# Performance work log

Hardware: AMD Instinct MI355X
Metric: run time of the kernel (lower is better)

Reference implementation:

```python
import jax, jax.numpy as jnp
import numpy as np

B, N, C = 2, 2048, 768
H = 12
HD = C // H
SCALE = HD ** -0.5


def setup_inputs() -> dict:
    key = jax.random.key(0)
    ks = jax.random.split(key, 5)
    s = 1.0 / np.sqrt(C)
    return {
        "x": jax.random.normal(ks[0], (B, N, C), dtype=jnp.float32),
        "Wq": jax.random.normal(ks[1], (C, C), dtype=jnp.float32) * s,
        "Wk": jax.random.normal(ks[2], (C, C), dtype=jnp.float32) * s,
        "Wv": jax.random.normal(ks[3], (C, C), dtype=jnp.float32) * s,
        "Wo": jax.random.normal(ks[4], (C, C), dtype=jnp.float32) * s,
        "bo": jnp.zeros((C,), dtype=jnp.float32),
    }


def reference(x, Wq, Wk, Wv, Wo, bo):
    b, n, c = x.shape
    # projections (equinox Linear: y = W @ x, i.e. x @ W.T); split heads -> [b, h, n, hd]
    q = (x @ Wq.T).reshape(b, n, H, HD).transpose(0, 2, 1, 3)
    k = (x @ Wk.T).reshape(b, n, H, HD).transpose(0, 2, 1, 3)
    v = (x @ Wv.T).reshape(b, n, H, HD).transpose(0, 2, 1, 3)
    # full O(N^2) score matrix, scaled dot-product
    scores = jnp.einsum("bhqd,bhkd->bhqk", q, k) * SCALE  # [b, h, n, n]
    probs = jax.nn.softmax(scores, axis=-1)
    # attn_drop = 0.0 -> identity
    out = jnp.einsum("bhqk,bhkd->bhqd", probs, v)  # [b, h, n, hd]
    out = out.transpose(0, 2, 1, 3).reshape(b, n, c)
    # output projection (proj_drop = 0.0 -> identity)
    return out @ Wo.T + bo
```

## Files before the change

kernel.cpp:

```cpp
#include <hip/hip_runtime.h>
#include <hip/hip_bf16.h>
#include <cstdint>

typedef __bf16 bf16;
typedef bf16 bf16x8 __attribute__((ext_vector_type(8)));
typedef float f32x4 __attribute__((ext_vector_type(4)));
typedef uint32_t u32;

#define MFMA16(a, b, c) __builtin_amdgcn_mfma_f32_16x16x32_bf16(a, b, c, 0, 0, 0)

static constexpr int Bb = 2, Hh = 12, Nn = 2048, Cc = 768, HD = 64;
static constexpr float SCALE_L2E = 0.125f * 1.4426950408889634f;

__device__ inline u32 pkbf(float a, float b) {
    union { struct { uint16_t lo, hi; } s; u32 w; } u;
    u.s.lo = __builtin_bit_cast(uint16_t, (bf16)a);
    u.s.hi = __builtin_bit_cast(uint16_t, (bf16)b);
    return u.w;
}

__device__ __forceinline__ size_t fidx(int bh, int n, int hd) {
    return ((size_t)(bh * 128 + (n >> 4)) * 2 + (hd >> 5)) * 512 +
           (size_t)(((hd >> 3) & 3) * 128 + (n & 15) * 8 + (hd & 7));
}
__device__ __forceinline__ size_t vidx(int bh, int n, int hd) {
    return (((size_t)(bh * 32 + (n >> 6)) * 4 + (hd >> 4)) * 2 + ((n >> 5) & 1)) * 512 +
           (size_t)(((n >> 3) & 3) * 128 + (hd & 15) * 8 + (n & 7));
}

__device__ __forceinline__ void stage16(const bf16* g, bf16* l) {
    __builtin_amdgcn_global_load_lds(
        (const __attribute__((address_space(1))) void*)g,
        (__attribute__((address_space(3))) void*)l, 16, 0, 0);
}

#define VMWAIT(N) do { asm volatile("s_waitcnt vmcnt(" #N ")" ::); \
                       __builtin_amdgcn_sched_barrier(0); } while (0)

#define GLD(dst, addr, off) \
    asm volatile("global_load_dwordx4 %0, %1, off offset:" #off \
                 : "=v"(dst) : "v"(addr))

#define CVTPK(w, a, b) \
    asm("v_cvt_pk_bf16_f32 %0, %1, %2" : "=v"(w) : "v"(a), "v"(b))

__global__ __launch_bounds__(256) void cvt_all(const float* __restrict__ x,
                                               const float* __restrict__ wq,
                                               const float* __restrict__ wk,
                                               const float* __restrict__ wv,
                                               const float* __restrict__ wo,
                                               bf16* __restrict__ xb,
                                               bf16* __restrict__ wqkv,
                                               bf16* __restrict__ wob) {
    const int b = blockIdx.x;
    const float* src;
    bf16* dst;
    int i;
    if (b < 1536) {
        src = x; dst = xb; i = b * 256 + threadIdx.x;
    } else {
        const int wbid  = b - 1536;
        const int which = wbid / 288;
        src = which == 0 ? wq : which == 1 ? wk : which == 2 ? wv : wo;
        dst = which == 3 ? wob : wqkv + (size_t)which * 589824;
        i = (wbid % 288) * 256 + threadIdx.x;
    }
    const float4* p = reinterpret_cast<const float4*>(src) + (size_t)i * 2;
    float4 v0 = p[0], v1 = p[1];
    bf16x8 o;
    o[0] = (bf16)v0.x; o[1] = (bf16)v0.y; o[2] = (bf16)v0.z; o[3] = (bf16)v0.w;
    o[4] = (bf16)v1.x; o[5] = (bf16)v1.y; o[6] = (bf16)v1.z; o[7] = (bf16)v1.w;
    reinterpret_cast<bf16x8*>(dst)[i] = o;
}

__global__ __launch_bounds__(256, 3) void gemm_qkv(const bf16* __restrict__ X,
                                                   const bf16* __restrict__ W,
                                                   bf16* __restrict__ QF,
                                                   bf16* __restrict__ KF,
                                                   bf16* __restrict__ VF) {
    const int m0      = blockIdx.x * 128;
    const int j00     = blockIdx.y * 128;
    const int grp     = blockIdx.y / 6;
    const int colbase = (blockIdx.y % 6) * 128;
    const int w   = threadIdx.x >> 6;
    const int wr  = w >> 1;
    const int wc  = w & 1;
    const int l   = threadIdx.x & 63;
    const int lr  = l & 15;
    const int lg  = l >> 4;

    __shared__ bf16 lsA[2][128 * 32];
    __shared__ bf16 lsB[2][128 * 32];

    const int lrow = l >> 2;
    const int lcol = (l & 3) * 8;

    auto STAGE = [&](int buf, int kk) {
#pragma unroll
        for (int i = 0; i < 2; i++) {
            const int s = w * 2 + i;
            stage16(X + (size_t)(m0 + s * 16 + lrow) * Cc + kk + lcol, &lsA[buf][s * 512]);
            stage16(W + (size_t)(j00 + s * 16 + lrow) * Cc + kk + lcol, &lsB[buf][s * 512]);
        }
    };

    f32x4 acc[4][4] = {};

    STAGE(0, 0);
    __syncthreads();
    int cur = 0;
#pragma unroll 1
    for (int it = 0; it < 24; ++it) {
        if (it < 23) STAGE(cur ^ 1, (it + 1) * 32);
        bf16x8 a[4], b[4];
#pragma unroll
        for (int r = 0; r < 4; r++)
            a[r] = *reinterpret_cast<const bf16x8*>(&lsA[cur][(wr * 64 + r * 16 + lr) * 32 + lg * 8]);
#pragma unroll
        for (int c = 0; c < 4; c++)
            b[c] = *reinterpret_cast<const bf16x8*>(&lsB[cur][(wc * 64 + c * 16 + lr) * 32 + lg * 8]);
        __builtin_amdgcn_s_setprio(1);
#pragma unroll
        for (int r = 0; r < 4; r++)
#pragma unroll
            for (int c = 0; c < 4; c++)
                acc[r][c] = MFMA16(a[r], b[c], acc[r][c]);
        __builtin_amdgcn_s_setprio(0);
        __syncthreads();
        cur ^= 1;
    }

#pragma unroll
    for (int r = 0; r < 4; r++)
#pragma unroll
        for (int c = 0; c < 4; c++)
#pragma unroll
            for (int j = 0; j < 4; j++) {
                const int m   = m0 + wr * 64 + r * 16 + lg * 4 + j;
                const int col = colbase + wc * 64 + c * 16 + lr;
                const int bb = m >> 11, n = m & 2047;
                const int h = col >> 6, hd = col & 63;
                const int bh = bb * Hh + h;
                const float v = acc[r][c][j];
                if (grp == 0) {
                    QF[fidx(bh, n, hd)] = (bf16)(v * SCALE_L2E);
                } else if (grp == 1) {
                    KF[fidx(bh, n, hd)] = (bf16)v;
                } else {
                    VF[vidx(bh, n, hd)] = (bf16)v;
                }
            }
}

__global__ __launch_bounds__(256) void gemm_proj(const bf16* __restrict__ X,
                                                 const bf16* __restrict__ W,
                                                 const float* __restrict__ bias,
                                                 float* __restrict__ Y) {
    const int m0 = blockIdx.x * 64;
    const int j0 = blockIdx.y * 64;
    const int w  = threadIdx.x >> 6;
    const int l  = threadIdx.x & 63;
    const int lr = l & 15;
    const int lg = l >> 4;

    __shared__ bf16 lsA[2][64 * 32];
    __shared__ bf16 lsB[2][64 * 32];

    const int lrow = l >> 2;
    const int lcol = (l & 3) * 8;

    auto STAGE = [&](int buf, int kk) {
        stage16(X + (size_t)(m0 + w * 16 + lrow) * Cc + kk + lcol, &lsA[buf][w * 512]);
        stage16(W + (size_t)(j0 + w * 16 + lrow) * Cc + kk + lcol, &lsB[buf][w * 512]);
    };

    f32x4 acc[4] = {};

    STAGE(0, 0);
    __syncthreads();
    int cur = 0;
#pragma unroll 1
    for (int it = 0; it < 24; ++it) {
        if (it < 23) STAGE(cur ^ 1, (it + 1) * 32);
        bf16x8 a = *reinterpret_cast<const bf16x8*>(&lsA[cur][(w * 16 + lr) * 32 + lg * 8]);
        bf16x8 b[4];
#pragma unroll
        for (int c = 0; c < 4; c++)
            b[c] = *reinterpret_cast<const bf16x8*>(&lsB[cur][(c * 16 + lr) * 32 + lg * 8]);
        __builtin_amdgcn_s_setprio(1);
#pragma unroll
        for (int c = 0; c < 4; c++)
            acc[c] = MFMA16(a, b[c], acc[c]);
        __builtin_amdgcn_s_setprio(0);
        __syncthreads();
        cur ^= 1;
    }

    const int mw = m0 + w * 16;
#pragma unroll
    for (int c = 0; c < 4; c++)
#pragma unroll
        for (int j = 0; j < 4; j++) {
            const int m   = mw + lg * 4 + j;
            const int col = j0 + c * 16 + lr;
            Y[(size_t)m * Cc + col] = acc[c][j] + bias[col];
        }
}

__global__ __launch_bounds__(256, 2) void attn_kernel(const bf16* __restrict__ QF,
                                                      const bf16* __restrict__ KF,
                                                      const bf16* __restrict__ VF,
                                                      bf16* __restrict__ AO) {
    const int bid  = (blockIdx.x & 7) * 96 + (blockIdx.x >> 3);
    const int qb   = bid & 31;
    const int bh   = bid >> 5;
    const int tid  = threadIdx.x;
    const int wid  = tid >> 6;
    const int team = wid >> 1;
    const int wt   = wid & 1;
    const int l    = tid & 63;
    const int lr   = l & 15;
    const int lg   = l >> 4;

    __shared__ u32 p_lds[4][2][576];

    f32x4 acc[2][4] = {};
    f32x4 accs[2] = {};

    const bf16* Qbase = QF + ((size_t)(bh * 128 + qb * 4 + wt * 2) * 2) * 512 + l * 8;
    const bf16x8 qa0 = *reinterpret_cast<const bf16x8*>(Qbase);
    const bf16x8 qb0 = *reinterpret_cast<const bf16x8*>(Qbase + 512);
    const bf16x8 qa1 = *reinterpret_cast<const bf16x8*>(Qbase + 1024);
    const bf16x8 qb1 = *reinterpret_cast<const bf16x8*>(Qbase + 1536);

    bf16x8 ONES;
#pragma unroll
    for (int i = 0; i < 8; i++) ONES[i] = (bf16)1.0f;

    bf16x8 ka[8], vv[8];
    const int tbase = team * 16;

    const bf16* kA = KF + ((size_t)bh * 256 + tbase * 8) * 512 + l * 8;
    const bf16* kB = kA + 2048;
    const bf16* vA = VF + ((size_t)bh * 256 + tbase * 8) * 512 + l * 8;
    const bf16* vB = vA + 2048;

    auto loadK = [&]() {
        GLD(ka[0], kA, 0);
        GLD(ka[1], kA, 1024);
        GLD(ka[2], kA, 2048);
        GLD(ka[3], kA, 3072);
        GLD(ka[4], kB, 0);
        GLD(ka[5], kB, 1024);
        GLD(ka[6], kB, 2048);
        GLD(ka[7], kB, 3072);
    };
    auto loadV = [&]() {
        GLD(vv[0], vA, 0);
        GLD(vv[1], vA, 1024);
        GLD(vv[2], vA, 2048);
        GLD(vv[3], vA, 3072);
        GLD(vv[4], vB, 0);
        GLD(vv[5], vB, 1024);
        GLD(vv[6], vB, 2048);
        GLD(vv[7], vB, 3072);
    };

    const f32x4 fz = {0.f, 0.f, 0.f, 0.f};

    auto EXPPACK = [&](int f, const f32x4* s) {
#pragma unroll
        for (int st = 0; st < 4; st++) {
            float e0 = exp2f(s[st][0]);
            float e1 = exp2f(s[st][1]);
            float e2 = exp2f(s[st][2]);
            float e3 = exp2f(s[st][3]);
            u32 w0, w1;
            CVTPK(w0, e0, e1);
            CVTPK(w1, e2, e3);
            *reinterpret_cast<uint2*>(&p_lds[wid][f][lr * 36 + st * 8 + lg * 2]) =
                make_uint2(w0, w1);
        }
    };

    loadK();
    loadV();

#pragma unroll 1
    for (int t = 0; t < 16; ++t) {
        VMWAIT(8);

        f32x4 s[4];
        __builtin_amdgcn_s_setprio(1);
#pragma unroll
        for (int st = 0; st < 4; st++) {
            s[st] = MFMA16(ka[st * 2], qa0, fz);
            s[st] = MFMA16(ka[st * 2 + 1], qb0, s[st]);
        }
        __builtin_amdgcn_s_setprio(0);
        EXPPACK(0, s);
        __builtin_amdgcn_s_setprio(1);
#pragma unroll
        for (int st = 0; st < 4; st++) {
            s[st] = MFMA16(ka[st * 2], qa1, fz);
            s[st] = MFMA16(ka[st * 2 + 1], qb1, s[st]);
        }
        __builtin_amdgcn_s_setprio(0);
        if (t < 15) {
            kA += 4096; kB += 4096;
            loadK();
        }
        EXPPACK(1, s);

        asm volatile("s_waitcnt lgkmcnt(0)" ::: "memory");
        __builtin_amdgcn_sched_barrier(0);
        const bf16x8 pa00 = *reinterpret_cast<const bf16x8*>(&p_lds[wid][0][lr * 36 + lg * 4]);
        const bf16x8 pa01 = *reinterpret_cast<const bf16x8*>(&p_lds[wid][0][lr * 36 + 16 + lg * 4]);
        const bf16x8 pa10 = *reinterpret_cast<const bf16x8*>(&p_lds[wid][1][lr * 36 + lg * 4]);
        const bf16x8 pa11 = *reinterpret_cast<const bf16x8*>(&p_lds[wid][1][lr * 36 + 16 + lg * 4]);

        VMWAIT(8);
        __builtin_amdgcn_s_setprio(1);
#pragma unroll
        for (int c = 0; c < 4; c++) {
            acc[0][c] = MFMA16(vv[c * 2], pa00, acc[0][c]);
            acc[0][c] = MFMA16(vv[c * 2 + 1], pa01, acc[0][c]);
            acc[1][c] = MFMA16(vv[c * 2], pa10, acc[1][c]);
            acc[1][c] = MFMA16(vv[c * 2 + 1], pa11, acc[1][c]);
        }
        accs[0] = MFMA16(ONES, pa00, accs[0]);
        accs[0] = MFMA16(ONES, pa01, accs[0]);
        accs[1] = MFMA16(ONES, pa10, accs[1]);
        accs[1] = MFMA16(ONES, pa11, accs[1]);
        __builtin_amdgcn_s_setprio(0);
        if (t < 15) {
            vA += 4096; vB += 4096;
            loadV();
        }
    }

    __syncthreads();
    float* mrg = reinterpret_cast<float*>(&p_lds[0][0][0]);
    if (team == 1) {
#pragma unroll
        for (int f = 0; f < 2; f++) {
            float* slot = mrg + (wt * 2 + f) * 1088 + l * 17;
#pragma unroll
            for (int c = 0; c < 4; c++)
#pragma unroll
                for (int j = 0; j < 4; j++) slot[c * 4 + j] = acc[f][c][j];
            slot[16] = accs[f][0];
        }
    }
    __syncthreads();
    if (team == 1) return;

    const int bb = bh / Hh, h = bh % Hh;
#pragma unroll
    for (int f = 0; f < 2; f++) {
        const float* slot = mrg + (wt * 2 + f) * 1088 + l * 17;
#pragma unroll
        for (int c = 0; c < 4; c++)
#pragma unroll
            for (int j = 0; j < 4; j++) acc[f][c][j] += slot[c * 4 + j];
        const float rtot = accs[f][0] + slot[16];
        const float rinv = 1.0f / rtot;
        asm volatile("s_waitcnt lgkmcnt(0)" ::: "memory");
        __builtin_amdgcn_sched_barrier(0);

        float* o_lds = mrg + (wt * 2 + f) * 1088;
#pragma unroll
        for (int c = 0; c < 4; c++)
#pragma unroll
            for (int j = 0; j < 4; j++)
                o_lds[(c * 16 + lg * 4 + j) * 17 + lr] = acc[f][c][j] * rinv;
        asm volatile("s_waitcnt lgkmcnt(0)" ::: "memory");
        __builtin_amdgcn_sched_barrier(0);

        const int q0 = qb * 64 + (wt * 2 + f) * 16;
        const int qq = l >> 2, dc = (l & 3) * 16;
        bf16x8 o0, o1;
#pragma unroll
        for (int dd = 0; dd < 8; dd++) o0[dd] = (bf16)o_lds[(dc + dd) * 17 + qq];
#pragma unroll
        for (int dd = 0; dd < 8; dd++) o1[dd] = (bf16)o_lds[(dc + 8 + dd) * 17 + qq];
        bf16* dst = AO + ((size_t)(bb * Nn) + q0 + qq) * Cc + h * 64 + dc;
        *reinterpret_cast<bf16x8*>(dst) = o0;
        *reinterpret_cast<bf16x8*>(dst + 8) = o1;
    }
}

extern "C" void kernel_launch(void* const* d_in, const int* in_sizes, int n_in,
                              void* d_out, int out_size, void* d_ws, size_t ws_size,
                              hipStream_t stream) {
    const float* x  = (const float*)d_in[0];
    const float* Wq = (const float*)d_in[1];
    const float* Wk = (const float*)d_in[2];
    const float* Wv = (const float*)d_in[3];
    const float* Wo = (const float*)d_in[4];
    const float* bo = (const float*)d_in[5];

    const size_t XB    = 0;
    const size_t WQKVB = XB + 6291456;
    const size_t WOB   = WQKVB + 3538944;
    const size_t QB    = WOB + 1179648;
    const size_t KB    = QB + 6291456;
    const size_t VTB   = KB + 6291456;
    const size_t AOB   = VTB + 6291456;
    const size_t NEED  = AOB + 6291456;
    if (ws_size < NEED) return;

    char* ws = (char*)d_ws;
    bf16* xb   = (bf16*)(ws + XB);
    bf16* wqkv = (bf16*)(ws + WQKVB);
    bf16* wob  = (bf16*)(ws + WOB);
    bf16* QF   = (bf16*)(ws + QB);
    bf16* KF   = (bf16*)(ws + KB);
    bf16* VF   = (bf16*)(ws + VTB);
    bf16* AOb  = (bf16*)(ws + AOB);

    cvt_all<<<2688, 256, 0, stream>>>(x, Wq, Wk, Wv, Wo, xb, wqkv, wob);

    gemm_qkv<<<dim3(32, 18), 256, 0, stream>>>(xb, wqkv, QF, KF, VF);

    attn_kernel<<<768, 256, 0, stream>>>(QF, KF, VF, AOb);

    gemm_proj<<<dim3(64, 12), 256, 0, stream>>>(AOb, wob, bo, (float*)d_out);
}
```

Baseline: 91.80 us.

## Switch attention to 32x32x16 MFMA and keep P in registers via permlane swap

Moves the attention kernel from 16x16x32 MFMA tiles to 32x32x16 tiles, rewriting the Q/K/V fragment layouts produced by the QKV GEMM. The exponentiated scores are packed to bf16 and rearranged across lane halves with v_permlane32_swap, so the P operand goes straight into the PV MFMA instead of round-tripping through LDS. The aim is to drop the per-iteration LDS writes, reads and waits and use fewer, larger MFMAs. The cost is higher register pressure from 16-wide accumulators, and correctness now rests on the new layout and swap mapping being exactly right.

```diff
diff --git a/kernel.cpp b/kernel.cpp
--- a/kernel.cpp
+++ b/kernel.cpp
@@ -5,27 +5,23 @@
 typedef __bf16 bf16;
 typedef bf16 bf16x8 __attribute__((ext_vector_type(8)));
 typedef float f32x4 __attribute__((ext_vector_type(4)));
+typedef float f32x16 __attribute__((ext_vector_type(16)));
 typedef uint32_t u32;
+typedef u32 u32x4 __attribute__((ext_vector_type(4)));
 
 #define MFMA16(a, b, c) __builtin_amdgcn_mfma_f32_16x16x32_bf16(a, b, c, 0, 0, 0)
+#define MFMA32(a, b, c) __builtin_amdgcn_mfma_f32_32x32x16_bf16(a, b, c, 0, 0, 0)
 
 static constexpr int Bb = 2, Hh = 12, Nn = 2048, Cc = 768, HD = 64;
 static constexpr float SCALE_L2E = 0.125f * 1.4426950408889634f;
 
-__device__ inline u32 pkbf(float a, float b) {
-    union { struct { uint16_t lo, hi; } s; u32 w; } u;
-    u.s.lo = __builtin_bit_cast(uint16_t, (bf16)a);
-    u.s.hi = __builtin_bit_cast(uint16_t, (bf16)b);
-    return u.w;
-}
-
-__device__ __forceinline__ size_t fidx(int bh, int n, int hd) {
-    return ((size_t)(bh * 128 + (n >> 4)) * 2 + (hd >> 5)) * 512 +
-           (size_t)(((hd >> 3) & 3) * 128 + (n & 15) * 8 + (hd & 7));
-}
-__device__ __forceinline__ size_t vidx(int bh, int n, int hd) {
-    return (((size_t)(bh * 32 + (n >> 6)) * 4 + (hd >> 4)) * 2 + ((n >> 5) & 1)) * 512 +
-           (size_t)(((n >> 3) & 3) * 128 + (hd & 15) * 8 + (n & 7));
+__device__ __forceinline__ size_t fidx32(int bh, int n, int hd) {
+    return ((size_t)(bh * 64 + (n >> 5)) * 4 + (hd >> 4)) * 512 +
+           (size_t)(((((hd >> 3) & 1) << 5) + (n & 31)) * 8 + (hd & 7));
+}
+__device__ __forceinline__ size_t vidx32(int bh, int n, int hd) {
+    return (((size_t)(bh * 32 + (n >> 6)) * 2 + (hd >> 5)) * 4 + ((n >> 4) & 3)) * 512 +
+           (size_t)(((((n >> 3) & 1) << 5) + (hd & 31)) * 8 + (n & 7));
 }
 
 __device__ __forceinline__ void stage16(const bf16* g, bf16* l) {
@@ -43,6 +39,9 @@
 
 #define CVTPK(w, a, b) \
     asm("v_cvt_pk_bf16_f32 %0, %1, %2" : "=v"(w) : "v"(a), "v"(b))
+
+#define PLSWAP(a, b) \
+    asm("v_permlane32_swap_b32 %0, %1" : "+v"(a), "+v"(b))
 
 __global__ __launch_bounds__(256) void cvt_all(const float* __restrict__ x,
                                                const float* __restrict__ wq,
@@ -143,11 +142,11 @@
                 const int bh = bb * Hh + h;
                 const float v = acc[r][c][j];
                 if (grp == 0) {
-                    QF[fidx(bh, n, hd)] = (bf16)(v * SCALE_L2E);
+                    QF[fidx32(bh, n, hd)] = (bf16)(v * SCALE_L2E);
                 } else if (grp == 1) {
-                    KF[fidx(bh, n, hd)] = (bf16)v;
+                    KF[fidx32(bh, n, hd)] = (bf16)v;
                 } else {
-                    VF[vidx(bh, n, hd)] = (bf16)v;
+                    VF[vidx32(bh, n, hd)] = (bf16)v;
                 }
             }
 }
@@ -219,19 +218,19 @@
     const int team = wid >> 1;
     const int wt   = wid & 1;
     const int l    = tid & 63;
-    const int lr   = l & 15;
-    const int lg   = l >> 4;
-
-    __shared__ u32 p_lds[4][2][576];
-
-    f32x4 acc[2][4] = {};
-    f32x4 accs[2] = {};
-
-    const bf16* Qbase = QF + ((size_t)(bh * 128 + qb * 4 + wt * 2) * 2) * 512 + l * 8;
-    const bf16x8 qa0 = *reinterpret_cast<const bf16x8*>(Qbase);
-    const bf16x8 qb0 = *reinterpret_cast<const bf16x8*>(Qbase + 512);
-    const bf16x8 qa1 = *reinterpret_cast<const bf16x8*>(Qbase + 1024);
-    const bf16x8 qb1 = *reinterpret_cast<const bf16x8*>(Qbase + 1536);
+    const int q    = l & 31;
+    const int hi   = l >> 5;
+
+    __shared__ float mrg[4224];
+
+    f32x16 acc0 = {}, acc1 = {};
+    f32x16 accs = {};
+
+    const bf16* Qp = QF + ((size_t)(bh * 64 + qb * 2 + wt) * 4) * 512 + l * 8;
+    bf16x8 qf[4];
+#pragma unroll
+    for (int dc = 0; dc < 4; dc++)
+        qf[dc] = *reinterpret_cast<const bf16x8*>(Qp + dc * 512);
 
     bf16x8 ONES;
 #pragma unroll
@@ -266,20 +265,24 @@
         GLD(vv[7], vB, 3072);
     };
 
-    const f32x4 fz = {0.f, 0.f, 0.f, 0.f};
-
-    auto EXPPACK = [&](int f, const f32x4* s) {
-#pragma unroll
-        for (int st = 0; st < 4; st++) {
-            float e0 = exp2f(s[st][0]);
-            float e1 = exp2f(s[st][1]);
-            float e2 = exp2f(s[st][2]);
-            float e3 = exp2f(s[st][3]);
-            u32 w0, w1;
-            CVTPK(w0, e0, e1);
-            CVTPK(w1, e2, e3);
-            *reinterpret_cast<uint2*>(&p_lds[wid][f][lr * 36 + st * 8 + lg * 2]) =
-                make_uint2(w0, w1);
+    const f32x16 fz16 = {};
+
+    auto BUILDB = [&](const f32x16& sP, bf16x8* Bw) {
+        float e[16];
+#pragma unroll
+        for (int r = 0; r < 16; r++) e[r] = exp2f(sP[r]);
+#pragma unroll
+        for (int c2 = 0; c2 < 2; c2++) {
+            u32 x0, x1, y0, y1;
+            CVTPK(x0, e[8 * c2 + 0], e[8 * c2 + 1]);
+            CVTPK(x1, e[8 * c2 + 2], e[8 * c2 + 3]);
+            CVTPK(y0, e[8 * c2 + 4], e[8 * c2 + 5]);
+            CVTPK(y1, e[8 * c2 + 6], e[8 * c2 + 7]);
+            PLSWAP(x0, y0);
+            PLSWAP(x1, y1);
+            u32x4 wv4;
+            wv4[0] = x0; wv4[1] = x1; wv4[2] = y0; wv4[3] = y1;
+            Bw[c2] = __builtin_bit_cast(bf16x8, wv4);
         }
     };
 
@@ -290,48 +293,32 @@
     for (int t = 0; t < 16; ++t) {
         VMWAIT(8);
 
-        f32x4 s[4];
+        bf16x8 Bw[4];
         __builtin_amdgcn_s_setprio(1);
-#pragma unroll
-        for (int st = 0; st < 4; st++) {
-            s[st] = MFMA16(ka[st * 2], qa0, fz);
-            s[st] = MFMA16(ka[st * 2 + 1], qb0, s[st]);
-        }
+        f32x16 s0 = fz16;
+#pragma unroll
+        for (int dc = 0; dc < 4; dc++) s0 = MFMA32(ka[dc], qf[dc], s0);
         __builtin_amdgcn_s_setprio(0);
-        EXPPACK(0, s);
+        BUILDB(s0, &Bw[0]);
         __builtin_amdgcn_s_setprio(1);
-#pragma unroll
-        for (int st = 0; st < 4; st++) {
-            s[st] = MFMA16(ka[st * 2], qa1, fz);
-            s[st] = MFMA16(ka[st * 2 + 1], qb1, s[st]);
-        }
+        f32x16 s1 = fz16;
+#pragma unroll
+        for (int dc = 0; dc < 4; dc++) s1 = MFMA32(ka[4 + dc], qf[dc], s1);
         __builtin_amdgcn_s_setprio(0);
         if (t < 15) {
             kA += 4096; kB += 4096;
             loadK();
         }
-        EXPPACK(1, s);
-
-        asm volatile("s_waitcnt lgkmcnt(0)" ::: "memory");
-        __builtin_amdgcn_sched_barrier(0);
-        const bf16x8 pa00 = *reinterpret_cast<const bf16x8*>(&p_lds[wid][0][lr * 36 + lg * 4]);
-        const bf16x8 pa01 = *reinterpret_cast<const bf16x8*>(&p_lds[wid][0][lr * 36 + 16 + lg * 4]);
-        const bf16x8 pa10 = *reinterpret_cast<const bf16x8*>(&p_lds[wid][1][lr * 36 + lg * 4]);
-        const bf16x8 pa11 = *reinterpret_cast<const bf16x8*>(&p_lds[wid][1][lr * 36 + 16 + lg * 4]);
-
-        VMWAIT(8);
+        BUILDB(s1, &Bw[2]);
+
+        if (t < 15) { VMWAIT(8); } else { VMWAIT(0); }
         __builtin_amdgcn_s_setprio(1);
 #pragma unroll
-        for (int c = 0; c < 4; c++) {
-            acc[0][c] = MFMA16(vv[c * 2], pa00, acc[0][c]);
-            acc[0][c] = MFMA16(vv[c * 2 + 1], pa01, acc[0][c]);
-            acc[1][c] = MFMA16(vv[c * 2], pa10, acc[1][c]);
-            acc[1][c] = MFMA16(vv[c * 2 + 1], pa11, acc[1][c]);
-        }
-        accs[0] = MFMA16(ONES, pa00, accs[0]);
-        accs[0] = MFMA16(ONES, pa01, accs[0]);
-        accs[1] = MFMA16(ONES, pa10, accs[1]);
-        accs[1] = MFMA16(ONES, pa11, accs[1]);
+        for (int kc = 0; kc < 4; kc++) {
+            acc0 = MFMA32(vv[kc], Bw[kc], acc0);
+            acc1 = MFMA32(vv[4 + kc], Bw[kc], acc1);
+            accs = MFMA32(ONES, Bw[kc], accs);
+        }
         __builtin_amdgcn_s_setprio(0);
         if (t < 15) {
             vA += 4096; vB += 4096;
@@ -340,53 +327,41 @@
     }
 
     __syncthreads();
-    float* mrg = reinterpret_cast<float*>(&p_lds[0][0][0]);
+    float* slot = mrg + wt * 2112 + l * 33;
     if (team == 1) {
 #pragma unroll
-        for (int f = 0; f < 2; f++) {
-            float* slot = mrg + (wt * 2 + f) * 1088 + l * 17;
-#pragma unroll
-            for (int c = 0; c < 4; c++)
-#pragma unroll
-                for (int j = 0; j < 4; j++) slot[c * 4 + j] = acc[f][c][j];
-            slot[16] = accs[f][0];
-        }
+        for (int r = 0; r < 16; r++) { slot[r] = acc0[r]; slot[16 + r] = acc1[r]; }
+        slot[32] = accs[0];
     }
     __syncthreads();
     if (team == 1) return;
 
+#pragma unroll
+    for (int r = 0; r < 16; r++) { acc0[r] += slot[r]; acc1[r] += slot[16 + r]; }
+    const float rinv = 1.0f / (accs[0] + slot[32]);
+    asm volatile("s_waitcnt lgkmcnt(0)" ::: "memory");
+    __builtin_amdgcn_sched_barrier(0);
+
+    float* o_lds = mrg + wt * 2112;
+#pragma unroll
+    for (int r = 0; r < 16; r++) {
+        const int d = (r & 3) + 8 * (r >> 2) + 4 * hi;
+        o_lds[d * 33 + q] = acc0[r] * rinv;
+        o_lds[(d + 32) * 33 + q] = acc1[r] * rinv;
+    }
+    asm volatile("s_waitcnt lgkmcnt(0)" ::: "memory");
+    __builtin_amdgcn_sched_barrier(0);
+
     const int bb = bh / Hh, h = bh % Hh;
-#pragma unroll
-    for (int f = 0; f < 2; f++) {
-        const float* slot = mrg + (wt * 2 + f) * 1088 + l * 17;
-#pragma unroll
-        for (int c = 0; c < 4; c++)
-#pragma unroll
-            for (int j = 0; j < 4; j++) acc[f][c][j] += slot[c * 4 + j];
-        const float rtot = accs[f][0] + slot[16];
-        const float rinv = 1.0f / rtot;
-        asm volatile("s_waitcnt lgkmcnt(0)" ::: "memory");
-        __builtin_amdgcn_sched_barrier(0);
-
-        float* o_lds = mrg + (wt * 2 + f) * 1088;
-#pragma unroll
-        for (int c = 0; c < 4; c++)
-#pragma unroll
-            for (int j = 0; j < 4; j++)
-                o_lds[(c * 16 + lg * 4 + j) * 17 + lr] = acc[f][c][j] * rinv;
-        asm volatile("s_waitcnt lgkmcnt(0)" ::: "memory");
-        __builtin_amdgcn_sched_barrier(0);
-
-        const int q0 = qb * 64 + (wt * 2 + f) * 16;
-        const int qq = l >> 2, dc = (l & 3) * 16;
-        bf16x8 o0, o1;
-#pragma unroll
-        for (int dd = 0; dd < 8; dd++) o0[dd] = (bf16)o_lds[(dc + dd) * 17 + qq];
-#pragma unroll
-        for (int dd = 0; dd < 8; dd++) o1[dd] = (bf16)o_lds[(dc + 8 + dd) * 17 + qq];
-        bf16* dst = AO + ((size_t)(bb * Nn) + q0 + qq) * Cc + h * 64 + dc;
-        *reinterpret_cast<bf16x8*>(dst) = o0;
-        *reinterpret_cast<bf16x8*>(dst + 8) = o1;
+    const int q0 = qb * 64 + wt * 32;
+    const int qq = l >> 1, dc0 = (l & 1) * 32;
+    bf16* dst = AO + ((size_t)(bb * Nn) + q0 + qq) * Cc + h * 64 + dc0;
+#pragma unroll
+    for (int d8 = 0; d8 < 4; d8++) {
+        bf16x8 o;
+#pragma unroll
+        for (int dd = 0; dd < 8; dd++) o[dd] = (bf16)o_lds[(dc0 + d8 * 8 + dd) * 33 + qq];
+        *reinterpret_cast<bf16x8*>(dst + d8 * 8) = o;
     }
 }
 
```

After: 97.16 us. 1.06x slower.

## Split attention keys across four waves with smaller query tiles and more blocks

Applied to the files above, without the earlier changes.

Each block now handles 32 queries instead of 64, and each of the four waves processes one quarter of the key range rather than two teams each covering half. Partial accumulators and row sums from three waves are merged through a dedicated LDS buffer, so the grid doubles to 1536 blocks and launch bounds request 5 blocks per SM. This is meant to raise occupancy and parallelism and shorten each wave's serial key loop. In exchange, K/V are loaded redundantly across more blocks and the serial cross-wave reduction is larger, with added LDS usage.

```diff
diff --git a/kernel.cpp b/kernel.cpp
--- a/kernel.cpp
+++ b/kernel.cpp
@@ -11,13 +11,6 @@
 
 static constexpr int Bb = 2, Hh = 12, Nn = 2048, Cc = 768, HD = 64;
 static constexpr float SCALE_L2E = 0.125f * 1.4426950408889634f;
-
-__device__ inline u32 pkbf(float a, float b) {
-    union { struct { uint16_t lo, hi; } s; u32 w; } u;
-    u.s.lo = __builtin_bit_cast(uint16_t, (bf16)a);
-    u.s.hi = __builtin_bit_cast(uint16_t, (bf16)b);
-    return u.w;
-}
 
 __device__ __forceinline__ size_t fidx(int bh, int n, int hd) {
     return ((size_t)(bh * 128 + (n >> 4)) * 2 + (hd >> 5)) * 512 +
@@ -207,27 +200,25 @@
         }
 }
 
-__global__ __launch_bounds__(256, 2) void attn_kernel(const bf16* __restrict__ QF,
+__global__ __launch_bounds__(256, 5) void attn_kernel(const bf16* __restrict__ QF,
                                                       const bf16* __restrict__ KF,
                                                       const bf16* __restrict__ VF,
                                                       bf16* __restrict__ AO) {
-    const int bid  = (blockIdx.x & 7) * 96 + (blockIdx.x >> 3);
-    const int qb   = bid & 31;
-    const int bh   = bid >> 5;
+    const int bid  = (blockIdx.x & 7) * 192 + (blockIdx.x >> 3);
+    const int qb   = bid & 63;
+    const int bh   = bid >> 6;
     const int tid  = threadIdx.x;
     const int wid  = tid >> 6;
-    const int team = wid >> 1;
-    const int wt   = wid & 1;
     const int l    = tid & 63;
     const int lr   = l & 15;
     const int lg   = l >> 4;
 
-    __shared__ u32 p_lds[4][2][576];
+    __shared__ float mrg[3 * 64 * 35];
 
     f32x4 acc[2][4] = {};
     f32x4 accs[2] = {};
 
-    const bf16* Qbase = QF + ((size_t)(bh * 128 + qb * 4 + wt * 2) * 2) * 512 + l * 8;
+    const bf16* Qbase = QF + ((size_t)(bh * 128 + qb * 2) * 2) * 512 + l * 8;
     const bf16x8 qa0 = *reinterpret_cast<const bf16x8*>(Qbase);
     const bf16x8 qb0 = *reinterpret_cast<const bf16x8*>(Qbase + 512);
     const bf16x8 qa1 = *reinterpret_cast<const bf16x8*>(Qbase + 1024);
@@ -238,7 +229,7 @@
     for (int i = 0; i < 8; i++) ONES[i] = (bf16)1.0f;
 
     bf16x8 ka[8], vv[8];
-    const int tbase = team * 16;
+    const int tbase = wid * 8;
 
     const bf16* kA = KF + ((size_t)bh * 256 + tbase * 8) * 512 + l * 8;
     const bf16* kB = kA + 2048;
@@ -268,6 +259,8 @@
 
     const f32x4 fz = {0.f, 0.f, 0.f, 0.f};
 
+    __shared__ u32 p_lds[4][2][576];
+
     auto EXPPACK = [&](int f, const f32x4* s) {
 #pragma unroll
         for (int st = 0; st < 4; st++) {
@@ -287,7 +280,7 @@
     loadV();
 
 #pragma unroll 1
-    for (int t = 0; t < 16; ++t) {
+    for (int t = 0; t < 8; ++t) {
         VMWAIT(8);
 
         f32x4 s[4];
@@ -306,7 +299,7 @@
             s[st] = MFMA16(ka[st * 2 + 1], qb1, s[st]);
         }
         __builtin_amdgcn_s_setprio(0);
-        if (t < 15) {
+        if (t < 7) {
             kA += 4096; kB += 4096;
             loadK();
         }
@@ -319,7 +312,7 @@
         const bf16x8 pa10 = *reinterpret_cast<const bf16x8*>(&p_lds[wid][1][lr * 36 + lg * 4]);
         const bf16x8 pa11 = *reinterpret_cast<const bf16x8*>(&p_lds[wid][1][lr * 36 + 16 + lg * 4]);
 
-        VMWAIT(8);
+        if (t < 7) { VMWAIT(8); } else { VMWAIT(0); }
         __builtin_amdgcn_s_setprio(1);
 #pragma unroll
         for (int c = 0; c < 4; c++) {
@@ -333,42 +326,48 @@
         accs[1] = MFMA16(ONES, pa10, accs[1]);
         accs[1] = MFMA16(ONES, pa11, accs[1]);
         __builtin_amdgcn_s_setprio(0);
-        if (t < 15) {
+        if (t < 7) {
             vA += 4096; vB += 4096;
             loadV();
         }
     }
 
     __syncthreads();
-    float* mrg = reinterpret_cast<float*>(&p_lds[0][0][0]);
-    if (team == 1) {
+    if (wid != 0) {
+        float* slot = mrg + (size_t)(wid - 1) * 64 * 35 + l * 35;
 #pragma unroll
         for (int f = 0; f < 2; f++) {
-            float* slot = mrg + (wt * 2 + f) * 1088 + l * 17;
 #pragma unroll
             for (int c = 0; c < 4; c++)
 #pragma unroll
-                for (int j = 0; j < 4; j++) slot[c * 4 + j] = acc[f][c][j];
-            slot[16] = accs[f][0];
+                for (int j = 0; j < 4; j++) slot[f * 16 + c * 4 + j] = acc[f][c][j];
+            slot[32 + f] = accs[f][0];
         }
     }
     __syncthreads();
-    if (team == 1) return;
+    if (wid != 0) return;
+
+    float rt[2] = {accs[0][0], accs[1][0]};
+#pragma unroll 1
+    for (int p = 0; p < 3; p++) {
+        const float* slot = mrg + (size_t)p * 64 * 35 + l * 35;
+#pragma unroll
+        for (int f = 0; f < 2; f++) {
+#pragma unroll
+            for (int c = 0; c < 4; c++)
+#pragma unroll
+                for (int j = 0; j < 4; j++) acc[f][c][j] += slot[f * 16 + c * 4 + j];
+            rt[f] += slot[32 + f];
+        }
+    }
+    asm volatile("s_waitcnt lgkmcnt(0)" ::: "memory");
+    __builtin_amdgcn_sched_barrier(0);
 
     const int bb = bh / Hh, h = bh % Hh;
 #pragma unroll
     for (int f = 0; f < 2; f++) {
-        const float* slot = mrg + (wt * 2 + f) * 1088 + l * 17;
-#pragma unroll
-        for (int c = 0; c < 4; c++)
-#pragma unroll
-            for (int j = 0; j < 4; j++) acc[f][c][j] += slot[c * 4 + j];
-        const float rtot = accs[f][0] + slot[16];
-        const float rinv = 1.0f / rtot;
-        asm volatile("s_waitcnt lgkmcnt(0)" ::: "memory");
-        __builtin_amdgcn_sched_barrier(0);
-
-        float* o_lds = mrg + (wt * 2 + f) * 1088;
+        const float rinv = 1.0f / rt[f];
+        float* o_lds = mrg + f * 1088;
 #pragma unroll
         for (int c = 0; c < 4; c++)
 #pragma unroll
@@ -377,7 +376,7 @@
         asm volatile("s_waitcnt lgkmcnt(0)" ::: "memory");
         __builtin_amdgcn_sched_barrier(0);
 
-        const int q0 = qb * 64 + (wt * 2 + f) * 16;
+        const int q0 = qb * 32 + f * 16;
         const int qq = l >> 2, dc = (l & 3) * 16;
         bf16x8 o0, o1;
 #pragma unroll
@@ -423,7 +422,7 @@
 
     gemm_qkv<<<dim3(32, 18), 256, 0, stream>>>(xb, wqkv, QF, KF, VF);
 
-    attn_kernel<<<768, 256, 0, stream>>>(QF, KF, VF, AOb);
+    attn_kernel<<<1536, 256, 0, stream>>>(QF, KF, VF, AOb);
 
     gemm_proj<<<dim3(64, 12), 256, 0, stream>>>(AOb, wob, bo, (float*)d_out);
 }
```

Measured after the change: 100.0 us. +9.0%, slower.
